# Kernel tuning notes

Measured on AMD Instinct MI355X. Metric: run time of the kernel, lower is better.

## Reference

```python
import math
import jax, jax.numpy as jnp
import numpy as np

NUM_PRE_NMS = 2000
NMS_THR = 0.7
MIN_SIZE = 16.0
LOG_MAX = math.log(1000.0 / 16)  # clamp on dh, dw as in the torch module

B, A, H, W = 8, 3, 200, 304
STRIDE = 4


def _make_anchors():
    # grid anchors, channel-last anchor ordering to match permute(0,2,3,1)
    sizes = np.array([32.0, 64.0, 128.0], dtype=np.float32)  # A sizes
    ys = (np.arange(H, dtype=np.float32) + 0.5) * STRIDE
    xs = (np.arange(W, dtype=np.float32) + 0.5) * STRIDE
    cy, cx = np.meshgrid(ys, xs, indexing="ij")  # [H,W]
    cx = cx[:, :, None]
    cy = cy[:, :, None]
    half = (sizes / 2.0)[None, None, :]  # [1,1,A]
    anc = np.stack([cx - half, cy - half, cx + half, cy + half], axis=-1)  # [H,W,A,4]
    anc = anc.reshape(-1, 4)  # [H*W*A, 4]
    anc = np.broadcast_to(anc[None], (B, anc.shape[0], 4)).copy()
    return jnp.asarray(anc)


def setup_inputs() -> dict:
    key = jax.random.key(0)
    k1, k2 = jax.random.split(key)
    cls_logits = jax.random.normal(k1, (B, A, H, W), dtype=jnp.float32)
    regs = jax.random.normal(k2, (B, 4 * A, H, W), dtype=jnp.float32) * 0.1
    anchors = _make_anchors()
    return {"cls_logits": cls_logits, "regs": regs, "anchors": anchors,
            "image_h": 800, "image_w": 1216}


def _box_iou(boxes):
    # boxes: [K,4] -> iou [K,K]
    x1, y1, x2, y2 = boxes[:, 0], boxes[:, 1], boxes[:, 2], boxes[:, 3]
    area = (x2 - x1) * (y2 - y1)
    ix1 = jnp.maximum(x1[:, None], x1[None, :])
    iy1 = jnp.maximum(y1[:, None], y1[None, :])
    ix2 = jnp.minimum(x2[:, None], x2[None, :])
    iy2 = jnp.minimum(y2[:, None], y2[None, :])
    iw = jnp.clip(ix2 - ix1, 0.0)
    ih = jnp.clip(iy2 - iy1, 0.0)
    inter = iw * ih
    union = area[:, None] + area[None, :] - inter
    return inter / jnp.maximum(union, 1e-6)


def _nms_one(boxes, valid):
    # boxes sorted by descending score; greedy suppression, fixed-size keep mask
    k = boxes.shape[0]
    iou = _box_iou(boxes)
    later = jnp.arange(k)

    def body(i, keep):
        sup = (iou[i] > NMS_THR) & keep[i] & (later > i)
        return keep & ~sup

    return jax.lax.fori_loop(0, k, body, valid)


def reference(cls_logits, regs, anchors, image_h, image_w):
    b = cls_logits.shape[0]
    # scores/regs in channel-last anchor order (matches permute(0,2,3,1))
    scores = jnp.transpose(cls_logits, (0, 2, 3, 1)).reshape(b, -1)       # [B,N]
    deltas = jnp.transpose(regs, (0, 2, 3, 1)).reshape(b, -1, 4)          # [B,N,4]
    n = scores.shape[1]
    k = min(NUM_PRE_NMS, n)

    top_scores, idx = jax.lax.top_k(scores, k)                            # [B,K]
    top_deltas = jnp.take_along_axis(deltas, idx[:, :, None], axis=1)     # [B,K,4]
    top_anchors = jnp.take_along_axis(anchors, idx[:, :, None], axis=1)   # [B,K,4]

    dx, dy = top_deltas[..., 0], top_deltas[..., 1]
    dh = jnp.minimum(top_deltas[..., 2], LOG_MAX)
    dw = jnp.minimum(top_deltas[..., 3], LOG_MAX)
    ah = top_anchors[..., 3] - top_anchors[..., 1]
    aw = top_anchors[..., 2] - top_anchors[..., 0]
    cx = aw / 2
    cy = ah / 2
    px = cx + dx * aw
    py = cy + dy * ah
    ph = jnp.exp(dh) * ah
    pw = jnp.exp(dw) * aw
    boxes = jnp.stack([px - pw / 2, py - ph / 2, px + pw / 2, py + ph / 2], axis=-1)  # [B,K,4]

    # size filter on clamped coords (as in _nms)
    w_img = jnp.float32(image_w)
    h_img = jnp.float32(image_h)
    bw = jnp.clip(boxes[..., 2], 0.0, w_img) - jnp.clip(boxes[..., 0], 0.0, w_img)
    bh = jnp.clip(boxes[..., 3], 0.0, h_img) - jnp.clip(boxes[..., 1], 0.0, h_img)
    valid = (bw >= MIN_SIZE) & (bh >= MIN_SIZE)

    keep = jax.vmap(_nms_one)(boxes, valid)                               # [B,K]
    out_boxes = boxes * keep[..., None].astype(boxes.dtype)
    return out_boxes, top_scores, keep
```

## Files before the change

kernel.cpp:

```cpp
#include <hip/hip_runtime.h>

#define HWSZ 60800
#define NA 3
#define NTOT 182400
#define KSEL 2000
#define CANDCAP 8192
#define NBATCH 8
#define GSPLIT 128
#define LOG_MAX_F 4.135166556742356f

#define OFF_H1    0
#define OFF_CCNT  65536
#define ZR_BYTES  65568
#define OFF_BOX   65568
#define OFF_VALID 321568
#define OFF_SUP   385568
#define OFF_CAND  385568
#define OFF_SUPT  4481568


__device__ __forceinline__ unsigned int xform(float f) {
    unsigned int b = __float_as_uint(f);
    return b ^ ((unsigned int)((int)b >> 31) | 0x80000000u);
}

__device__ __forceinline__ void bar_lds() {
    asm volatile("s_waitcnt lgkmcnt(0)" ::: "memory");
    __builtin_amdgcn_s_barrier();
}

__global__ __launch_bounds__(256) void k_hist1(const float* __restrict__ cls,
                                               unsigned int* __restrict__ hist1) {
    int b = blockIdx.y, part = blockIdx.x, tid = threadIdx.x;
    __shared__ unsigned int h[2048];
    for (int i = tid; i < 2048; i += 256) h[i] = 0u;
    __syncthreads();
    const float4* base4 = (const float4*)(cls + (size_t)b * NTOT);
    const int n4 = NTOT / 4;
    int per = (n4 + GSPLIT - 1) / GSPLIT;
    int lo = part * per, hi = lo + per;
    if (hi > n4) hi = n4;
    for (int i = lo + tid; i < hi; i += 256) {
        float4 v = base4[i];
        atomicAdd(&h[xform(v.x) >> 21], 1u);
        atomicAdd(&h[xform(v.y) >> 21], 1u);
        atomicAdd(&h[xform(v.z) >> 21], 1u);
        atomicAdd(&h[xform(v.w) >> 21], 1u);
    }
    __syncthreads();
    unsigned int* gh = hist1 + b * 2048;
    for (int i = tid; i < 2048; i += 256)
        if (h[i]) atomicAdd(&gh[i], h[i]);
}

__global__ __launch_bounds__(256) void k_gather(const float* __restrict__ cls,
                                                const unsigned int* __restrict__ hist1,
                                                unsigned long long* __restrict__ cand,
                                                unsigned int* __restrict__ ccnt) {
    int b = blockIdx.y, part = blockIdx.x, tid = threadIdx.x;
    __shared__ unsigned int sa[2048], sb[2048];
    __shared__ unsigned long long lbuf[1024];
    __shared__ unsigned int lcnt, gbase, sbin;

    const unsigned int* gh = hist1 + b * 2048;
    #pragma unroll
    for (int k = 0; k < 8; ++k) {
        int i = tid + k * 256;
        sa[i] = gh[i];
    }
    if (tid == 0) lcnt = 0u;
    unsigned int* src = sa; unsigned int* dst = sb;
    for (int d = 1; d < 2048; d <<= 1) {
        __syncthreads();
        #pragma unroll
        for (int k = 0; k < 8; ++k) {
            int i = tid + k * 256;
            dst[i] = src[i] + ((i + d < 2048) ? src[i + d] : 0u);
        }
        unsigned int* t = src; src = dst; dst = t;
    }
    __syncthreads();
    #pragma unroll
    for (int k = 0; k < 8; ++k) {
        int i = tid + k * 256;
        unsigned int c = src[i];
        unsigned int cn = (i < 2047) ? src[i + 1] : 0u;
        if (c >= KSEL && cn < KSEL) sbin = (unsigned int)i;
    }
    __syncthreads();
    unsigned int bin = sbin;

    const float4* base4 = (const float4*)(cls + (size_t)b * NTOT);
    const int n4 = NTOT / 4;
    int per = (n4 + GSPLIT - 1) / GSPLIT;
    int lo = part * per, hi = lo + per;
    if (hi > n4) hi = n4;
    for (int i = lo + tid; i < hi; i += 256) {
        float4 v = base4[i];
        float vals[4] = {v.x, v.y, v.z, v.w};
        int idx0 = i * 4;
        #pragma unroll
        for (int q = 0; q < 4; ++q) {
            unsigned int u = xform(vals[q]);
            if ((u >> 21) >= bin) {
                int idx = idx0 + q;
                int a = idx / HWSZ;
                int hw = idx - a * HWSZ;
                unsigned int n = (unsigned int)(hw * NA + a);
                unsigned int pos = atomicAdd(&lcnt, 1u);
                if (pos < 1024u)
                    lbuf[pos] = ((unsigned long long)u << 32) | (unsigned long long)(~n);
            }
        }
    }
    __syncthreads();
    if (tid == 0) {
        unsigned int c = lcnt < 1024u ? lcnt : 1024u;
        gbase = atomicAdd(&ccnt[b], c);
    }
    __syncthreads();
    unsigned int c = lcnt < 1024u ? lcnt : 1024u;
    unsigned int gb = gbase;
    for (unsigned int i = tid; i < c; i += 256) {
        unsigned int p = gb + i;
        if (p < CANDCAP) cand[(size_t)b * CANDCAP + p] = lbuf[i];
    }
}

__global__ __launch_bounds__(256) void k_rank_decode(
        const unsigned long long* __restrict__ cand,
        const unsigned int* __restrict__ ccnt,
        const float* __restrict__ regs,
        const float* __restrict__ anchors,
        const int* __restrict__ img_h,
        const int* __restrict__ img_w,
        float* __restrict__ out_scores,
        float4* __restrict__ boxes_ws,
        unsigned int* __restrict__ valid_ws) {
    int b = blockIdx.y;
    int tid = threadIdx.x;
    unsigned int sc = ccnt[b];
    if (sc > CANDCAP) sc = CANDCAP;
    unsigned int kbase = blockIdx.x * 64;
    if (kbase >= sc) return;
    int ki = tid & 63;
    int q = tid >> 6;
    int lane = tid & 63;
    const unsigned long long* sb_ = cand + (size_t)b * CANDCAP;
    unsigned int r = kbase + (unsigned int)ki;
    unsigned long long mykey = (r < sc) ? sb_[r] : 0ULL;

    unsigned int qs = ((sc + 255u) >> 8) << 6;
    unsigned int lo = (unsigned int)q * qs;
    unsigned int hi = lo + qs;
    if (hi > sc) hi = sc;

    unsigned int cnt = 0u;
    for (unsigned int base = lo; base < hi; base += 64) {
        unsigned long long kj = 0ULL;
        if (base + (unsigned int)lane < hi) kj = sb_[base + lane];
        unsigned int klo = (unsigned int)kj;
        unsigned int khi = (unsigned int)(kj >> 32);
        #pragma unroll
        for (int t = 0; t < 64; ++t) {
            unsigned int lo_ = (unsigned int)__builtin_amdgcn_readlane((int)klo, t);
            unsigned int hi_ = (unsigned int)__builtin_amdgcn_readlane((int)khi, t);
            unsigned long long kt = ((unsigned long long)hi_ << 32) | (unsigned long long)lo_;
            cnt += (kt > mykey) ? 1u : 0u;
        }
    }
    __shared__ unsigned int cntsh[4][64];
    cntsh[q][ki] = cnt;
    __syncthreads();
    if (tid >= 64) return;
    unsigned int rank = cntsh[0][ki] + cntsh[1][ki] + cntsh[2][ki] + cntsh[3][ki];
    if (r >= sc || rank >= KSEL) return;

    int hv = img_h[0];
    int wv = img_w[0];
    float himg = (hv > 0 && hv < 100000) ? (float)hv : __int_as_float(hv);
    float wimg = (wv > 0 && wv < 100000) ? (float)wv : __int_as_float(wv);

    unsigned int u = (unsigned int)(mykey >> 32);
    unsigned int n = ~((unsigned int)mykey);
    unsigned int bits = (u & 0x80000000u) ? (u & 0x7FFFFFFFu) : ~u;
    float score = __uint_as_float(bits);
    int a = (int)(n % NA);
    int hw = (int)(n / NA);
    const float* rp = regs + ((size_t)b * (4 * NA) + 4 * a) * HWSZ + hw;
    float dx = rp[0 * HWSZ];
    float dy = rp[1 * HWSZ];
    float dh = rp[2 * HWSZ];
    float dw = rp[3 * HWSZ];
    const float* ap = anchors + ((size_t)b * NTOT + n) * 4;
    float ax1 = ap[0], ay1 = ap[1], ax2 = ap[2], ay2 = ap[3];
    float ahh = ay2 - ay1;
    float aww = ax2 - ax1;
    float cx = aww * 0.5f;
    float cy = ahh * 0.5f;
    float px = cx + dx * aww;
    float py = cy + dy * ahh;
    dh = fminf(dh, LOG_MAX_F);
    dw = fminf(dw, LOG_MAX_F);
    float ph = expf(dh) * ahh;
    float pw = expf(dw) * aww;
    float x1 = px - pw * 0.5f;
    float y1 = py - ph * 0.5f;
    float x2 = px + pw * 0.5f;
    float y2 = py + ph * 0.5f;
    float bwv = fminf(fmaxf(x2, 0.f), wimg) - fminf(fmaxf(x1, 0.f), wimg);
    float bhv = fminf(fmaxf(y2, 0.f), himg) - fminf(fmaxf(y1, 0.f), himg);
    unsigned int valid = (bwv >= 16.f && bhv >= 16.f) ? 1u : 0u;
    size_t o = (size_t)b * KSEL + rank;
    out_scores[o] = score;
    boxes_ws[o] = make_float4(x1, y1, x2, y2);
    valid_ws[o] = valid;
}

__global__ __launch_bounds__(256) void k_supmat(const float4* __restrict__ boxes_ws,
                                                unsigned long long* __restrict__ sup,
                                                unsigned long long* __restrict__ supT) {
    int ct = blockIdx.x;
    int rt = blockIdx.y;
    int b  = blockIdx.z;
    if (ct * 64 + 63 < rt * 256) return;
    int tid = threadIdx.x;
    __shared__ float4 colbox[64];
    int j0 = ct * 64;
    if (tid < 64) {
        int jl = j0 + tid;
        colbox[tid] = (jl < KSEL) ? boxes_ws[(size_t)b * KSEL + jl]
                                  : make_float4(0.f, 0.f, 0.f, 0.f);
    }
    __syncthreads();
    int i = rt * 256 + tid;
    if (i >= KSEL) return;
    float4 bi = boxes_ws[(size_t)b * KSEL + i];
    float area_i = (bi.z - bi.x) * (bi.w - bi.y);
    unsigned long long word = 0ULL;
    #pragma unroll 8
    for (int jj = 0; jj < 64; ++jj) {
        int j = j0 + jj;
        float4 bj = colbox[jj];
        float area_j = (bj.z - bj.x) * (bj.w - bj.y);
        float ix1 = fmaxf(bi.x, bj.x);
        float iy1 = fmaxf(bi.y, bj.y);
        float ix2 = fminf(bi.z, bj.z);
        float iy2 = fminf(bi.w, bj.w);
        float iw = fmaxf(ix2 - ix1, 0.f);
        float ih = fmaxf(iy2 - iy1, 0.f);
        float inter = iw * ih;
        float uni = area_i + area_j - inter;
        float iou = inter / fmaxf(uni, 1e-6f);
        bool s = (j > i) && (j < KSEL) && (iou > 0.7f);
        if (s) word |= (1ULL << jj);
    }
    if (ct >= (i >> 6))
        sup[((size_t)b * KSEL + i) * 32 + ct] = word;

    if (ct == rt * 4 + (tid >> 6)) {
        int lane = tid & 63;
        unsigned long long cm = 0ULL;
        #pragma unroll
        for (int j = 0; j < 64; ++j) {
            unsigned long long t = __ballot((word >> j) & 1ULL);
            if (lane == j) cm = t;
        }
        supT[((size_t)b * 32 + ct) * 64 + lane] = cm;
    }
}

#define LOAD_TILE(wnext, buf)                                                \
    {                                                                        \
        int w_ = (wnext);                                                    \
        unsigned long long pe_ =                                             \
            ((unsigned long long)accw[w_ * 2 + 1] << 32)                     \
            | (unsigned long long)accw[w_ * 2];                              \
        unsigned long long est_ = kws[w_] & ~pe_;                            \
        _Pragma("unroll")                                                    \
        for (int k = 0; k < 4; ++k) {                                        \
            int lr_ = (tid >> 4) + k * 16;                                   \
            int grow_ = w_ * 64 + lr_;                                       \
            if (!((est_ >> lr_) & 1ULL)) grow_ = w_ * 64;                    \
            int pp_ = (2 * p + 1 >= w_) ? p : 15;                            \
            buf[k] = srowp[(size_t)grow_ * 16 + pp_];                        \
        }                                                                    \
    }

#define PROCESS_TILE(w, buf)                                                 \
    {                                                                        \
        bar_lds();                                                           \
        int w_ = (w);                                                        \
        unsigned long long pend_ =                                           \
            ((unsigned long long)accw[w_ * 2 + 1] << 32)                     \
            | (unsigned long long)accw[w_ * 2];                              \
        unsigned long long cand_ = kws[w_] & ~pend_;                         \
        unsigned int clo_ = __builtin_amdgcn_readfirstlane((unsigned int)cand_);        \
        unsigned int chi_ = __builtin_amdgcn_readfirstlane((unsigned int)(cand_ >> 32));\
        unsigned long long cur_ = ((unsigned long long)chi_ << 32)           \
                                  | (unsigned long long)clo_;                \
        if (cur_) {                                                          \
            unsigned long long cmw_ = colT[w_ * 64 + lane];                  \
            unsigned long long k_ = cur_;                                    \
            for (;;) {                                                       \
                unsigned long long sup_ = __ballot((k_ & cmw_) != 0ULL);     \
                unsigned long long k2_ = cur_ & ~sup_;                       \
                if (k2_ == k_) break;                                        \
                k_ = k2_;                                                    \
            }                                                                \
            cur_ = k_;                                                       \
            if (tid == 0) fin[w_] = cur_;                                    \
            unsigned long long v0_ = 0ULL, v1_ = 0ULL;                       \
            _Pragma("unroll")                                                \
            for (int k = 0; k < 4; ++k) {                                    \
                int lr_ = (tid >> 4) + k * 16;                               \
                if ((cur_ >> lr_) & 1ULL) { v0_ |= buf[k].x; v1_ |= buf[k].y; } \
            }                                                                \
            v0_ |= __shfl_xor(v0_, 16, 64); v0_ |= __shfl_xor(v0_, 32, 64);  \
            v1_ |= __shfl_xor(v1_, 16, 64); v1_ |= __shfl_xor(v1_, 32, 64);  \
            if (lane < 16) {                                                 \
                int wd0_ = 2 * p;                                            \
                if (wd0_ > w_ && v0_) {                                      \
                    atomicOr(&accw[wd0_ * 2], (unsigned int)v0_);            \
                    atomicOr(&accw[wd0_ * 2 + 1], (unsigned int)(v0_ >> 32));\
                }                                                            \
                if (wd0_ + 1 > w_ && v1_) {                                  \
                    atomicOr(&accw[wd0_ * 2 + 2], (unsigned int)v1_);        \
                    atomicOr(&accw[wd0_ * 2 + 3], (unsigned int)(v1_ >> 32));\
                }                                                            \
            }                                                                \
        } else if (tid == 0) {                                               \
            fin[w_] = 0ULL;                                                  \
        }                                                                    \
    }

__global__ __launch_bounds__(256) void k_nms_scan(const unsigned long long* __restrict__ sup,
                                                  const unsigned long long* __restrict__ supT,
                                                  const unsigned int* __restrict__ valid_ws,
                                                  const float4* __restrict__ boxes_ws,
                                                  float* __restrict__ out_boxes,
                                                  float* __restrict__ out_keep) {
    int b = blockIdx.x;
    int tid = threadIdx.x;
    int lane = tid & 63;
    int p = tid & 15;
    __shared__ unsigned long long kws[32];
    __shared__ unsigned long long fin[32];
    __shared__ unsigned int accw[64];
    __shared__ unsigned long long colT[32 * 64];
    const ulonglong2* srowp = (const ulonglong2*)(sup + (size_t)b * KSEL * 32);

    {
        const unsigned long long* stb = supT + (size_t)b * 2048;
        #pragma unroll
        for (int k = 0; k < 8; ++k) {
            int i = tid + k * 256;
            colT[i] = stb[i];
        }
    }

    if (tid < 32) {
        unsigned long long kw = 0ULL;
        const uint4* vv = (const uint4*)(valid_ws + (size_t)b * KSEL);
        #pragma unroll 4
        for (int q = 0; q < 16; ++q) {
            uint4 x = vv[tid * 16 + q];
            int base = q * 4;
            if (x.x) kw |= 1ULL << (base + 0);
            if (x.y) kw |= 1ULL << (base + 1);
            if (x.z) kw |= 1ULL << (base + 2);
            if (x.w) kw |= 1ULL << (base + 3);
        }
        if (tid == 31) kw &= 0xFFFFULL;
        kws[tid] = kw;
    }
    if (tid < 64) accw[tid] = 0u;
    bar_lds();

    ulonglong2 A[4], B[4], C[4], D[4];
    LOAD_TILE(0, A);
    LOAD_TILE(1, B);
    LOAD_TILE(2, C);
    LOAD_TILE(3, D);

    for (int t = 0; t < 8; ++t) {
        int w = 4 * t;
        PROCESS_TILE(w, A);
        if (w + 4 < 32) LOAD_TILE(w + 4, A);
        PROCESS_TILE(w + 1, B);
        if (w + 5 < 32) LOAD_TILE(w + 5, B);
        PROCESS_TILE(w + 2, C);
        if (w + 6 < 32) LOAD_TILE(w + 6, C);
        PROCESS_TILE(w + 3, D);
        if (w + 7 < 32) LOAD_TILE(w + 7, D);
    }
    bar_lds();

    float4* ob4 = (float4*)out_boxes;
    for (int r = tid; r < KSEL; r += 256) {
        float kf = (float)((fin[r >> 6] >> (r & 63)) & 1ULL);
        size_t o = (size_t)b * KSEL + r;
        out_keep[o] = kf;
        float4 bx = boxes_ws[o];
        ob4[o] = make_float4(bx.x * kf, bx.y * kf, bx.z * kf, bx.w * kf);
    }
}

extern "C" void kernel_launch(void* const* d_in, const int* in_sizes, int n_in,
                              void* d_out, int out_size, void* d_ws, size_t ws_size,
                              hipStream_t stream) {
    const float* cls     = (const float*)d_in[0];
    const float* regs    = (const float*)d_in[1];
    const float* anchors = (const float*)d_in[2];
    const int*   img_h   = (const int*)d_in[3];
    const int*   img_w   = (const int*)d_in[4];

    float* out = (float*)d_out;
    float* out_boxes  = out;
    float* out_scores = out + 64000;
    float* out_keep   = out + 80000;

    char* ws = (char*)d_ws;
    unsigned int* hist1      = (unsigned int*)(ws + OFF_H1);
    unsigned int* ccnt       = (unsigned int*)(ws + OFF_CCNT);
    float4* boxes_ws         = (float4*)(ws + OFF_BOX);
    unsigned int* valid_ws   = (unsigned int*)(ws + OFF_VALID);
    unsigned long long* sup  = (unsigned long long*)(ws + OFF_SUP);
    unsigned long long* cand = (unsigned long long*)(ws + OFF_CAND);
    unsigned long long* supT = (unsigned long long*)(ws + OFF_SUPT);

    hipMemsetAsync(ws, 0, ZR_BYTES, stream);
    k_hist1<<<dim3(GSPLIT, NBATCH), 256, 0, stream>>>(cls, hist1);
    k_gather<<<dim3(GSPLIT, NBATCH), 256, 0, stream>>>(cls, hist1, cand, ccnt);
    k_rank_decode<<<dim3(CANDCAP / 64, NBATCH), 256, 0, stream>>>(cand, ccnt, regs, anchors,
                                                                  img_h, img_w, out_scores,
                                                                  boxes_ws, valid_ws);
    k_supmat<<<dim3(32, 8, NBATCH), 256, 0, stream>>>(boxes_ws, sup, supT);
    k_nms_scan<<<NBATCH, 256, 0, stream>>>(sup, supT, valid_ws, boxes_ws, out_boxes, out_keep);
}
```

Baseline: 202.1 us.

## Run NMS scan on a single wavefront to eliminate per-tile block barriers

The serial NMS scan now runs on one 64-lane wavefront instead of four wavefronts synchronised with a block barrier per 64-box tile. Each lane holds 16 rows per tile in registers, and rows are no longer masked by the estimated candidate set before loading. This removes 32 barriers per batch, but each lane issues four times as many loads, and register use grows (launch bounds set to one block per CU), so unroll pressure and register spills are a risk.

```diff
diff --git a/kernel.cpp b/kernel.cpp
--- a/kernel.cpp
+++ b/kernel.cpp
@@ -22,11 +22,6 @@
 __device__ __forceinline__ unsigned int xform(float f) {
     unsigned int b = __float_as_uint(f);
     return b ^ ((unsigned int)((int)b >> 31) | 0x80000000u);
-}
-
-__device__ __forceinline__ void bar_lds() {
-    asm volatile("s_waitcnt lgkmcnt(0)" ::: "memory");
-    __builtin_amdgcn_s_barrier();
 }
 
 __global__ __launch_bounds__(256) void k_hist1(const float* __restrict__ cls,
@@ -270,26 +265,21 @@
     }
 }
 
-#define LOAD_TILE(wnext, buf)                                                \
+#define LOAD_T1(wnext, buf)                                                  \
     {                                                                        \
         int w_ = (wnext);                                                    \
-        unsigned long long pe_ =                                             \
-            ((unsigned long long)accw[w_ * 2 + 1] << 32)                     \
-            | (unsigned long long)accw[w_ * 2];                              \
-        unsigned long long est_ = kws[w_] & ~pe_;                            \
         _Pragma("unroll")                                                    \
-        for (int k = 0; k < 4; ++k) {                                        \
-            int lr_ = (tid >> 4) + k * 16;                                   \
+        for (int k = 0; k < 16; ++k) {                                       \
+            int lr_ = slot + k * 4;                                          \
             int grow_ = w_ * 64 + lr_;                                       \
-            if (!((est_ >> lr_) & 1ULL)) grow_ = w_ * 64;                    \
+            if (grow_ > KSEL - 1) grow_ = KSEL - 1;                          \
             int pp_ = (2 * p + 1 >= w_) ? p : 15;                            \
             buf[k] = srowp[(size_t)grow_ * 16 + pp_];                        \
         }                                                                    \
     }
 
-#define PROCESS_TILE(w, buf)                                                 \
+#define PROC_T1(w, buf)                                                      \
     {                                                                        \
-        bar_lds();                                                           \
         int w_ = (w);                                                        \
         unsigned long long pend_ =                                           \
             ((unsigned long long)accw[w_ * 2 + 1] << 32)                     \
@@ -309,11 +299,11 @@
                 k_ = k2_;                                                    \
             }                                                                \
             cur_ = k_;                                                       \
-            if (tid == 0) fin[w_] = cur_;                                    \
+            if (lane == 0) fin[w_] = cur_;                                   \
             unsigned long long v0_ = 0ULL, v1_ = 0ULL;                       \
             _Pragma("unroll")                                                \
-            for (int k = 0; k < 4; ++k) {                                    \
-                int lr_ = (tid >> 4) + k * 16;                               \
+            for (int k = 0; k < 16; ++k) {                                   \
+                int lr_ = slot + k * 4;                                      \
                 if ((cur_ >> lr_) & 1ULL) { v0_ |= buf[k].x; v1_ |= buf[k].y; } \
             }                                                                \
             v0_ |= __shfl_xor(v0_, 16, 64); v0_ |= __shfl_xor(v0_, 32, 64);  \
@@ -329,21 +319,21 @@
                     atomicOr(&accw[wd0_ * 2 + 3], (unsigned int)(v1_ >> 32));\
                 }                                                            \
             }                                                                \
-        } else if (tid == 0) {                                               \
+        } else if (lane == 0) {                                              \
             fin[w_] = 0ULL;                                                  \
         }                                                                    \
     }
 
-__global__ __launch_bounds__(256) void k_nms_scan(const unsigned long long* __restrict__ sup,
-                                                  const unsigned long long* __restrict__ supT,
-                                                  const unsigned int* __restrict__ valid_ws,
-                                                  const float4* __restrict__ boxes_ws,
-                                                  float* __restrict__ out_boxes,
-                                                  float* __restrict__ out_keep) {
+__global__ __launch_bounds__(256, 1) void k_nms_scan(
+        const unsigned long long* __restrict__ sup,
+        const unsigned long long* __restrict__ supT,
+        const unsigned int* __restrict__ valid_ws,
+        const float4* __restrict__ boxes_ws,
+        float* __restrict__ out_boxes,
+        float* __restrict__ out_keep) {
     int b = blockIdx.x;
     int tid = threadIdx.x;
     int lane = tid & 63;
-    int p = tid & 15;
     __shared__ unsigned long long kws[32];
     __shared__ unsigned long long fin[32];
     __shared__ unsigned int accw[64];
@@ -358,7 +348,6 @@
             colT[i] = stb[i];
         }
     }
-
     if (tid < 32) {
         unsigned long long kw = 0ULL;
         const uint4* vv = (const uint4*)(valid_ws + (size_t)b * KSEL);
@@ -375,26 +364,29 @@
         kws[tid] = kw;
     }
     if (tid < 64) accw[tid] = 0u;
-    bar_lds();
-
-    ulonglong2 A[4], B[4], C[4], D[4];
-    LOAD_TILE(0, A);
-    LOAD_TILE(1, B);
-    LOAD_TILE(2, C);
-    LOAD_TILE(3, D);
-
-    for (int t = 0; t < 8; ++t) {
-        int w = 4 * t;
-        PROCESS_TILE(w, A);
-        if (w + 4 < 32) LOAD_TILE(w + 4, A);
-        PROCESS_TILE(w + 1, B);
-        if (w + 5 < 32) LOAD_TILE(w + 5, B);
-        PROCESS_TILE(w + 2, C);
-        if (w + 6 < 32) LOAD_TILE(w + 6, C);
-        PROCESS_TILE(w + 3, D);
-        if (w + 7 < 32) LOAD_TILE(w + 7, D);
-    }
-    bar_lds();
+    __syncthreads();
+
+    if (tid < 64) {
+        int slot = lane >> 4;
+        int p = lane & 15;
+        ulonglong2 A[16], B[16], C[16], D[16];
+        LOAD_T1(0, A);
+        LOAD_T1(1, B);
+        LOAD_T1(2, C);
+        LOAD_T1(3, D);
+        #pragma unroll
+        for (int t = 0; t < 8; ++t) {
+            PROC_T1(4 * t + 0, A);
+            if (4 * t + 4 < 32) LOAD_T1(4 * t + 4, A);
+            PROC_T1(4 * t + 1, B);
+            if (4 * t + 5 < 32) LOAD_T1(4 * t + 5, B);
+            PROC_T1(4 * t + 2, C);
+            if (4 * t + 6 < 32) LOAD_T1(4 * t + 6, C);
+            PROC_T1(4 * t + 3, D);
+            if (4 * t + 7 < 32) LOAD_T1(4 * t + 7, D);
+        }
+    }
+    __syncthreads();
 
     float4* ob4 = (float4*)out_boxes;
     for (int r = tid; r < KSEL; r += 256) {
```

Result: slower. 224.6 us (+11.1%).
